# Performance work log

Hardware: AMD Instinct MI355X
Metric: run time of the kernel (lower is better)

Reference implementation:

```python
import jax, jax.numpy as jnp
import numpy as np

N, D, E = 100000, 128, 800000

def setup_inputs() -> dict:
    key = jax.random.key(0)
    k1, k2, k3, k4 = jax.random.split(key, 4)
    z = jax.random.normal(k1, (N, D), dtype=jnp.float32)
    edge_index = jax.random.randint(k2, (2, E), 0, N, dtype=jnp.int64)
    # PyTorch-style init scale for Linear layers (kaiming-uniform-ish via normal is fine for a numeric reference)
    W1 = jax.random.normal(k3, (2 * D, D), dtype=jnp.float32) * (1.0 / np.sqrt(2 * D))
    b1 = jnp.zeros((D,), dtype=jnp.float32)
    W2 = jax.random.normal(k4, (D, 1), dtype=jnp.float32) * (1.0 / np.sqrt(D))
    b2 = jnp.zeros((1,), dtype=jnp.float32)
    return {"z": z, "edge_index": edge_index, "W1": W1, "b1": b1, "W2": W2, "b2": b2}

def reference(z, edge_index, W1, b1, W2, b2):
    # row/col gather of node embeddings
    row, col = edge_index[0], edge_index[1]
    # cat([z[row], z[col]]) @ W1 == z[row] @ W1[:D] + z[col] @ W1[D:]
    # -> avoids materializing the [E, 2D] concatenated tensor
    d = z.shape[1]
    h = z[row] @ W1[:d] + z[col] @ W1[d:] + b1          # [E, D]
    h = jax.nn.relu(h)                                   # Dropout(0.1) is identity in eval mode
    out = h @ W2 + b2                                    # [E, 1]
    return out.squeeze(-1)                               # [E]
```

## Files before the change

### kernel.cpp

```cpp
#include <hip/hip_runtime.h>

#define DDIM 128

typedef __bf16 bf16x8 __attribute__((ext_vector_type(8)));
typedef float  floatx4 __attribute__((ext_vector_type(4)));

__device__ inline unsigned short f2bf(float f) {
    unsigned u = __builtin_bit_cast(unsigned, f);
    u += 0x7fffu + ((u >> 16) & 1u);
    return (unsigned short)(u >> 16);
}

__global__ __launch_bounds__(256) void swizzle_w(
    const float* __restrict__ W1, unsigned short* __restrict__ Wf)
{
    const int id   = blockIdx.x * 256 + threadIdx.x;
    const int f    = id >> 6;
    const int lane = id & 63;
    const int nt = f >> 2, ks = f & 3;
    const int n  = nt * 16 + (lane & 15);
    const int kb = ks * 32 + (lane >> 4) * 8;
    const float* __restrict__ wsrc = (n < DDIM)
        ? (W1 + (size_t)kb * DDIM + n)
        : (W1 + (size_t)(DDIM + kb) * DDIM + (n - DDIM));
    unsigned short frag[8];
    #pragma unroll
    for (int j = 0; j < 8; ++j)
        frag[j] = f2bf(wsrc[(size_t)j * DDIM]);
    *(uint4*)&Wf[(size_t)id * 8] = *(const uint4*)frag;
}

__global__ __launch_bounds__(256, 3) void precompute_uv_mfma_q8(
    const float* __restrict__ z, const unsigned short* __restrict__ Wf,
    const float* __restrict__ b1,
    signed char* __restrict__ U8, signed char* __restrict__ V8,
    float* __restrict__ u_scale, float* __restrict__ v_scale,
    int N)
{
    const int lane = threadIdx.x & 63;
    const int w    = threadIdx.x >> 6;
    const int mrow = lane & 15;
    const int quad = lane >> 4;
    const int m0   = blockIdx.x * 64 + w * 16;

    bf16x8 afrag[4];
    {
        int grow = m0 + mrow; if (grow > N - 1) grow = N - 1;
        const float* zrow = z + (size_t)grow * DDIM;
        #pragma unroll
        for (int ks = 0; ks < 4; ++ks) {
            const int k0 = ks * 32 + quad * 8;
            const float4 x0 = *(const float4*)(zrow + k0);
            const float4 x1 = *(const float4*)(zrow + k0 + 4);
            unsigned short a[8];
            a[0] = f2bf(x0.x); a[1] = f2bf(x0.y); a[2] = f2bf(x0.z); a[3] = f2bf(x0.w);
            a[4] = f2bf(x1.x); a[5] = f2bf(x1.y); a[6] = f2bf(x1.z); a[7] = f2bf(x1.w);
            afrag[ks] = __builtin_bit_cast(bf16x8, *(const uint4*)a);
        }
    }

    #pragma unroll
    for (int half = 0; half < 2; ++half) {
        signed char* __restrict__ dst8 = half ? V8 : U8;
        float*       __restrict__ dscl = half ? v_scale : u_scale;

        float bval[8];
        #pragma unroll
        for (int nt = 0; nt < 8; ++nt)
            bval[nt] = half ? 0.f : b1[nt * 16 + mrow];

        floatx4 acc[8];
        #pragma unroll
        for (int nt = 0; nt < 8; ++nt) acc[nt] = (floatx4){0.f, 0.f, 0.f, 0.f};

        const unsigned short* __restrict__ wbase =
            Wf + ((size_t)half * 32 * 64) * 8 + (size_t)lane * 8;

        #pragma unroll
        for (int ks = 0; ks < 4; ++ks) {
            #pragma unroll
            for (int nt = 0; nt < 8; ++nt) {
                const bf16x8 b = __builtin_bit_cast(bf16x8,
                    *(const uint4*)(wbase + (size_t)((nt * 4 + ks) * 64) * 8));
                acc[nt] = __builtin_amdgcn_mfma_f32_16x16x32_bf16(afrag[ks], b, acc[nt], 0, 0, 0);
            }
        }

        #pragma unroll
        for (int r = 0; r < 4; ++r) {
            float mx = 0.f;
            #pragma unroll
            for (int nt = 0; nt < 8; ++nt)
                mx = fmaxf(mx, fabsf(acc[nt][r] + bval[nt]));
            #pragma unroll
            for (int m = 1; m < 16; m <<= 1)
                mx = fmaxf(mx, __shfl_xor(mx, m, 16));
            mx = fmaxf(mx, 1e-20f);
            const float inv = 127.f / mx;

            unsigned char bytes[8];
            #pragma unroll
            for (int nt = 0; nt < 8; ++nt) {
                const int q = (int)rintf((acc[nt][r] + bval[nt]) * inv);
                bytes[nt] = (unsigned char)(q & 0xff);
            }
            const int grow = m0 + quad * 4 + r;
            if (grow < N) {
                *(unsigned long long*)&dst8[(size_t)grow * DDIM + mrow * 8] =
                    *(const unsigned long long*)bytes;
                if (mrow == 0) dscl[grow] = mx * (1.f / 127.f);
            }
        }
    }
}

__global__ __launch_bounds__(256) void edge_kernel_i8(
    const int* __restrict__ ei,
    const signed char* __restrict__ U8, const signed char* __restrict__ V8,
    const float* __restrict__ u_scale, const float* __restrict__ v_scale,
    const float* __restrict__ W2, const float* __restrict__ b2,
    float* __restrict__ out, int E)
{
    const int t  = threadIdx.x;
    const int p  = t & 15;
    const int g0 = (blockIdx.x * 16 + (t >> 4)) * 4;

    float ww[8];
    #pragma unroll
    for (int j = 0; j < 8; ++j) ww[j] = W2[j * 16 + p];

    if (g0 >= E) return;

    int rows[4], cols[4];
    if (g0 + 3 < E) {
        const int4 r4 = *(const int4*)(ei + g0);
        const int4 c4 = *(const int4*)(ei + (size_t)E + g0);
        rows[0]=r4.x; rows[1]=r4.y; rows[2]=r4.z; rows[3]=r4.w;
        cols[0]=c4.x; cols[1]=c4.y; cols[2]=c4.z; cols[3]=c4.w;
    } else {
        #pragma unroll
        for (int i = 0; i < 4; ++i) {
            const int gi = (g0 + i < E) ? (g0 + i) : (E - 1);
            rows[i] = ei[gi];
            cols[i] = ei[(size_t)E + gi];
        }
    }

    uint2 uu[4], vv[4];
    #pragma unroll
    for (int i = 0; i < 4; ++i)
        uu[i] = *(const uint2*)(U8 + (size_t)rows[i] * DDIM + p * 8);
    #pragma unroll
    for (int i = 0; i < 4; ++i)
        vv[i] = *(const uint2*)(V8 + (size_t)cols[i] * DDIM + p * 8);

    float su[4], sv[4];
    #pragma unroll
    for (int i = 0; i < 4; ++i) { su[i] = u_scale[rows[i]]; sv[i] = v_scale[cols[i]]; }

    const float bias = b2[0];

    #pragma unroll
    for (int i = 0; i < 4; ++i) {
        const signed char* us = (const signed char*)&uu[i];
        const signed char* vs = (const signed char*)&vv[i];
        float s = 0.f;
        #pragma unroll
        for (int j = 0; j < 8; ++j) {
            const float h = fmaf(sv[i], (float)vs[j], su[i] * (float)us[j]);
            s = fmaf(fmaxf(h, 0.f), ww[j], s);
        }
        #pragma unroll
        for (int off = 8; off > 0; off >>= 1)
            s += __shfl_down(s, off, 16);
        if (p == 0 && g0 + i < E) out[g0 + i] = s + bias;
    }
}

__global__ __launch_bounds__(256) void edge_fused_fallback(
    const float* __restrict__ z, const int* __restrict__ ei,
    const float* __restrict__ W1, const float* __restrict__ b1,
    const float* __restrict__ W2, const float* __restrict__ b2,
    float* __restrict__ out, int N, int E)
{
    const int tid  = blockIdx.x * 256 + threadIdx.x;
    const int e    = tid >> 6;
    const int lane = tid & 63;
    if (e >= E) return;

    const int row = ei[e];
    const int col = ei[(size_t)E + e];
    const float* zr = z + (size_t)row * DDIM;
    const float* zc = z + (size_t)col * DDIM;

    float h0 = b1[lane];
    float h1 = b1[lane + 64];
    for (int k = 0; k < DDIM; ++k) {
        const float a = zr[k];
        const float b = zc[k];
        h0 = fmaf(a, W1[k * DDIM + lane],               h0);
        h0 = fmaf(b, W1[(DDIM + k) * DDIM + lane],      h0);
        h1 = fmaf(a, W1[k * DDIM + lane + 64],          h1);
        h1 = fmaf(b, W1[(DDIM + k) * DDIM + lane + 64], h1);
    }
    float s = fmaxf(h0, 0.f) * W2[lane] + fmaxf(h1, 0.f) * W2[lane + 64];
    #pragma unroll
    for (int off = 32; off > 0; off >>= 1)
        s += __shfl_down(s, off, 64);
    if (lane == 0) out[e] = s + b2[0];
}

extern "C" void kernel_launch(void* const* d_in, const int* in_sizes, int n_in,
                              void* d_out, int out_size, void* d_ws, size_t ws_size,
                              hipStream_t stream)
{
    const float* z  = (const float*)d_in[0];
    const int*   ei = (const int*)d_in[1];
    const float* W1 = (const float*)d_in[2];
    const float* b1 = (const float*)d_in[3];
    const float* W2 = (const float*)d_in[4];
    const float* b2 = (const float*)d_in[5];
    float*       out = (float*)d_out;

    const int N = in_sizes[0] / DDIM;
    const int E = in_sizes[1] / 2;

    const size_t n128 = (size_t)N * DDIM;
    const size_t need = 2 * n128 + 2 * (size_t)N * sizeof(float)
                      + 64 * 1024 + 512;
    if (ws_size >= need) {
        signed char* U8 = (signed char*)d_ws;
        signed char* V8 = U8 + n128;
        float* usc = (float*)(((size_t)(V8 + n128) + 255) & ~(size_t)255);
        float* vsc = usc + N;
        unsigned short* Wf = (unsigned short*)(((size_t)(vsc + N) + 255) & ~(size_t)255);

        hipLaunchKernelGGL(swizzle_w, dim3(16), dim3(256), 0, stream, W1, Wf);
        hipLaunchKernelGGL(precompute_uv_mfma_q8, dim3((N + 63) / 64), dim3(256), 0, stream,
                           z, Wf, b1, U8, V8, usc, vsc, N);
        hipLaunchKernelGGL(edge_kernel_i8, dim3((E + 63) / 64), dim3(256), 0, stream,
                           ei, U8, V8, usc, vsc, W2, b2, out, E);
    } else {
        hipLaunchKernelGGL(edge_fused_fallback, dim3((E + 3) / 4), dim3(256), 0, stream,
                           z, ei, W1, b1, W2, b2, out, N, E);
    }
}
```

Before: 146.7 us.

## Switch node precompute to 32x32x16 MFMA tiles with 32 rows per wave

The node-level U/V precompute moves from 16x16x32 bf16 MFMA to 32x32x16 bf16 MFMA. Each wave now handles 32 rows and a block handles 128 nodes. The weight swizzle, the quantized output layout (4 bytes per lane, interleaved columns) and the W2 indexing in the edge kernel are all changed to match. The goal is fewer MFMA issues and weight loads per row, with better reuse of each B fragment. In exchange the grid is halved, accumulators grow to 64 VGPRs, and the per-lane int8 stores become narrower.

```diff
diff --git a/kernel.cpp b/kernel.cpp
--- a/kernel.cpp
+++ b/kernel.cpp
@@ -2,8 +2,8 @@
 
 #define DDIM 128
 
-typedef __bf16 bf16x8 __attribute__((ext_vector_type(8)));
-typedef float  floatx4 __attribute__((ext_vector_type(4)));
+typedef __bf16 bf16x8  __attribute__((ext_vector_type(8)));
+typedef float  floatx16 __attribute__((ext_vector_type(16)));
 
 __device__ inline unsigned short f2bf(float f) {
     unsigned u = __builtin_bit_cast(unsigned, f);
@@ -17,9 +17,9 @@
     const int id   = blockIdx.x * 256 + threadIdx.x;
     const int f    = id >> 6;
     const int lane = id & 63;
-    const int nt = f >> 2, ks = f & 3;
-    const int n  = nt * 16 + (lane & 15);
-    const int kb = ks * 32 + (lane >> 4) * 8;
+    const int ct = f >> 3, s = f & 7;
+    const int n  = ct * 32 + (lane & 31);
+    const int kb = s * 16 + (lane >> 5) * 8;
     const float* __restrict__ wsrc = (n < DDIM)
         ? (W1 + (size_t)kb * DDIM + n)
         : (W1 + (size_t)(DDIM + kb) * DDIM + (n - DDIM));
@@ -39,23 +39,23 @@
 {
     const int lane = threadIdx.x & 63;
     const int w    = threadIdx.x >> 6;
-    const int mrow = lane & 15;
-    const int quad = lane >> 4;
-    const int m0   = blockIdx.x * 64 + w * 16;
-
-    bf16x8 afrag[4];
+    const int c    = lane & 31;
+    const int h    = lane >> 5;
+    const int m0   = blockIdx.x * 128 + w * 32;
+
+    bf16x8 afrag[8];
     {
-        int grow = m0 + mrow; if (grow > N - 1) grow = N - 1;
+        int grow = m0 + c; if (grow > N - 1) grow = N - 1;
         const float* zrow = z + (size_t)grow * DDIM;
         #pragma unroll
-        for (int ks = 0; ks < 4; ++ks) {
-            const int k0 = ks * 32 + quad * 8;
+        for (int s = 0; s < 8; ++s) {
+            const int k0 = s * 16 + h * 8;
             const float4 x0 = *(const float4*)(zrow + k0);
             const float4 x1 = *(const float4*)(zrow + k0 + 4);
             unsigned short a[8];
             a[0] = f2bf(x0.x); a[1] = f2bf(x0.y); a[2] = f2bf(x0.z); a[3] = f2bf(x0.w);
             a[4] = f2bf(x1.x); a[5] = f2bf(x1.y); a[6] = f2bf(x1.z); a[7] = f2bf(x1.w);
-            afrag[ks] = __builtin_bit_cast(bf16x8, *(const uint4*)a);
+            afrag[s] = __builtin_bit_cast(bf16x8, *(const uint4*)a);
         }
     }
 
@@ -64,51 +64,53 @@
         signed char* __restrict__ dst8 = half ? V8 : U8;
         float*       __restrict__ dscl = half ? v_scale : u_scale;
 
-        float bval[8];
-        #pragma unroll
-        for (int nt = 0; nt < 8; ++nt)
-            bval[nt] = half ? 0.f : b1[nt * 16 + mrow];
-
-        floatx4 acc[8];
-        #pragma unroll
-        for (int nt = 0; nt < 8; ++nt) acc[nt] = (floatx4){0.f, 0.f, 0.f, 0.f};
-
-        const unsigned short* __restrict__ wbase =
-            Wf + ((size_t)half * 32 * 64) * 8 + (size_t)lane * 8;
-
-        #pragma unroll
-        for (int ks = 0; ks < 4; ++ks) {
-            #pragma unroll
-            for (int nt = 0; nt < 8; ++nt) {
+        float bval[4];
+        #pragma unroll
+        for (int ct = 0; ct < 4; ++ct)
+            bval[ct] = half ? 0.f : b1[ct * 32 + c];
+
+        floatx16 acc[4];
+        #pragma unroll
+        for (int ct = 0; ct < 4; ++ct)
+            #pragma unroll
+            for (int q = 0; q < 16; ++q) acc[ct][q] = 0.f;
+
+        #pragma unroll
+        for (int s = 0; s < 8; ++s) {
+            #pragma unroll
+            for (int ct = 0; ct < 4; ++ct) {
+                const int f = (half * 4 + ct) * 8 + s;
                 const bf16x8 b = __builtin_bit_cast(bf16x8,
-                    *(const uint4*)(wbase + (size_t)((nt * 4 + ks) * 64) * 8));
-                acc[nt] = __builtin_amdgcn_mfma_f32_16x16x32_bf16(afrag[ks], b, acc[nt], 0, 0, 0);
+                    *(const uint4*)&Wf[((size_t)f * 64 + lane) * 8]);
+                acc[ct] = __builtin_amdgcn_mfma_f32_32x32x16_bf16(afrag[s], b, acc[ct], 0, 0, 0);
             }
         }
 
         #pragma unroll
-        for (int r = 0; r < 4; ++r) {
-            float mx = 0.f;
-            #pragma unroll
-            for (int nt = 0; nt < 8; ++nt)
-                mx = fmaxf(mx, fabsf(acc[nt][r] + bval[nt]));
-            #pragma unroll
-            for (int m = 1; m < 16; m <<= 1)
-                mx = fmaxf(mx, __shfl_xor(mx, m, 16));
+        for (int q = 0; q < 16; ++q) {
+            float v[4];
+            #pragma unroll
+            for (int ct = 0; ct < 4; ++ct) v[ct] = acc[ct][q] + bval[ct];
+
+            float mx = fmaxf(fmaxf(fabsf(v[0]), fabsf(v[1])),
+                             fmaxf(fabsf(v[2]), fabsf(v[3])));
+            #pragma unroll
+            for (int m = 1; m < 32; m <<= 1)
+                mx = fmaxf(mx, __shfl_xor(mx, m, 32));
             mx = fmaxf(mx, 1e-20f);
             const float inv = 127.f / mx;
 
-            unsigned char bytes[8];
-            #pragma unroll
-            for (int nt = 0; nt < 8; ++nt) {
-                const int q = (int)rintf((acc[nt][r] + bval[nt]) * inv);
-                bytes[nt] = (unsigned char)(q & 0xff);
-            }
-            const int grow = m0 + quad * 4 + r;
+            unsigned char bytes[4];
+            #pragma unroll
+            for (int ct = 0; ct < 4; ++ct)
+                bytes[ct] = (unsigned char)(((int)rintf(v[ct] * inv)) & 0xff);
+
+            const int lrow = (q & 3) + 8 * (q >> 2) + 4 * h;
+            const int grow = m0 + lrow;
             if (grow < N) {
-                *(unsigned long long*)&dst8[(size_t)grow * DDIM + mrow * 8] =
-                    *(const unsigned long long*)bytes;
-                if (mrow == 0) dscl[grow] = mx * (1.f / 127.f);
+                *(unsigned int*)&dst8[(size_t)grow * DDIM + c * 4] =
+                    *(const unsigned int*)bytes;
+                if (c == 0) dscl[grow] = mx * (1.f / 127.f);
             }
         }
     }
@@ -127,7 +129,7 @@
 
     float ww[8];
     #pragma unroll
-    for (int j = 0; j < 8; ++j) ww[j] = W2[j * 16 + p];
+    for (int j = 0; j < 8; ++j) ww[j] = W2[(j & 3) * 32 + 2 * p + (j >> 2)];
 
     if (g0 >= E) return;
 
@@ -236,7 +238,7 @@
         unsigned short* Wf = (unsigned short*)(((size_t)(vsc + N) + 255) & ~(size_t)255);
 
         hipLaunchKernelGGL(swizzle_w, dim3(16), dim3(256), 0, stream, W1, Wf);
-        hipLaunchKernelGGL(precompute_uv_mfma_q8, dim3((N + 63) / 64), dim3(256), 0, stream,
+        hipLaunchKernelGGL(precompute_uv_mfma_q8, dim3((N + 127) / 128), dim3(256), 0, stream,
                            z, Wf, b1, U8, V8, usc, vsc, N);
         hipLaunchKernelGGL(edge_kernel_i8, dim3((E + 63) / 64), dim3(256), 0, stream,
                            ei, U8, V8, usc, vsc, W2, b2, out, E);
```

Result: slower. 152.6 us (+4.0%).

## Make node precompute kernel persistent with prefetch of next chunk's z rows

Applied to the files above, without the earlier changes.

The per-node U/V precompute kernel becomes a grid-stride persistent kernel with 512 blocks. Each block prefetches the next 64-row chunk of z into registers while it runs the MFMA and quantisation for the current chunk. The half loop is no longer unrolled and the bias loads are hoisted out of the loop. The aim is to hide global load latency for z behind compute, at the cost of more register pressure from the prefetch buffers, which may lower occupancy.

```diff
diff --git a/kernel.cpp b/kernel.cpp
--- a/kernel.cpp
+++ b/kernel.cpp
@@ -19,7 +19,7 @@
     const int lane = id & 63;
     const int nt = f >> 2, ks = f & 3;
     const int n  = nt * 16 + (lane & 15);
-    const int kb = ks * 32 + (lane >> 4) * 8;
+    const int kb = ks * 32 + ((lane >> 4) & 3) * 8;
     const float* __restrict__ wsrc = (n < DDIM)
         ? (W1 + (size_t)kb * DDIM + n)
         : (W1 + (size_t)(DDIM + kb) * DDIM + (n - DDIM));
@@ -35,82 +35,116 @@
     const float* __restrict__ b1,
     signed char* __restrict__ U8, signed char* __restrict__ V8,
     float* __restrict__ u_scale, float* __restrict__ v_scale,
-    int N)
+    int N, int nchunks)
 {
     const int lane = threadIdx.x & 63;
     const int w    = threadIdx.x >> 6;
     const int mrow = lane & 15;
     const int quad = lane >> 4;
-    const int m0   = blockIdx.x * 64 + w * 16;
-
-    bf16x8 afrag[4];
+
+    float bu[8];
+    #pragma unroll
+    for (int nt = 0; nt < 8; ++nt) bu[nt] = b1[nt * 16 + mrow];
+
+    int chunk = blockIdx.x;
+    if (chunk >= nchunks) return;
+
+    const int koff = quad * 8;
+
+    float4 raw[8];
     {
-        int grow = m0 + mrow; if (grow > N - 1) grow = N - 1;
+        int grow = chunk * 64 + w * 16 + mrow; if (grow > N - 1) grow = N - 1;
         const float* zrow = z + (size_t)grow * DDIM;
         #pragma unroll
         for (int ks = 0; ks < 4; ++ks) {
-            const int k0 = ks * 32 + quad * 8;
-            const float4 x0 = *(const float4*)(zrow + k0);
-            const float4 x1 = *(const float4*)(zrow + k0 + 4);
+            raw[ks * 2]     = *(const float4*)(zrow + ks * 32 + koff);
+            raw[ks * 2 + 1] = *(const float4*)(zrow + ks * 32 + koff + 4);
+        }
+    }
+
+    while (true) {
+        const int next = chunk + gridDim.x;
+        const bool have_next = next < nchunks;
+
+        bf16x8 afrag[4];
+        #pragma unroll
+        for (int ks = 0; ks < 4; ++ks) {
+            const float4 x0 = raw[ks * 2], x1 = raw[ks * 2 + 1];
             unsigned short a[8];
             a[0] = f2bf(x0.x); a[1] = f2bf(x0.y); a[2] = f2bf(x0.z); a[3] = f2bf(x0.w);
             a[4] = f2bf(x1.x); a[5] = f2bf(x1.y); a[6] = f2bf(x1.z); a[7] = f2bf(x1.w);
             afrag[ks] = __builtin_bit_cast(bf16x8, *(const uint4*)a);
         }
-    }
-
-    #pragma unroll
-    for (int half = 0; half < 2; ++half) {
-        signed char* __restrict__ dst8 = half ? V8 : U8;
-        float*       __restrict__ dscl = half ? v_scale : u_scale;
-
-        float bval[8];
-        #pragma unroll
-        for (int nt = 0; nt < 8; ++nt)
-            bval[nt] = half ? 0.f : b1[nt * 16 + mrow];
-
-        floatx4 acc[8];
-        #pragma unroll
-        for (int nt = 0; nt < 8; ++nt) acc[nt] = (floatx4){0.f, 0.f, 0.f, 0.f};
-
-        const unsigned short* __restrict__ wbase =
-            Wf + ((size_t)half * 32 * 64) * 8 + (size_t)lane * 8;
-
-        #pragma unroll
-        for (int ks = 0; ks < 4; ++ks) {
-            #pragma unroll
-            for (int nt = 0; nt < 8; ++nt) {
-                const bf16x8 b = __builtin_bit_cast(bf16x8,
-                    *(const uint4*)(wbase + (size_t)((nt * 4 + ks) * 64) * 8));
-                acc[nt] = __builtin_amdgcn_mfma_f32_16x16x32_bf16(afrag[ks], b, acc[nt], 0, 0, 0);
+
+        float4 raw2[8];
+        if (have_next) {
+            int grow = next * 64 + w * 16 + mrow; if (grow > N - 1) grow = N - 1;
+            const float* zrow = z + (size_t)grow * DDIM;
+            #pragma unroll
+            for (int ks = 0; ks < 4; ++ks) {
+                raw2[ks * 2]     = *(const float4*)(zrow + ks * 32 + koff);
+                raw2[ks * 2 + 1] = *(const float4*)(zrow + ks * 32 + koff + 4);
             }
         }
 
-        #pragma unroll
-        for (int r = 0; r < 4; ++r) {
-            float mx = 0.f;
-            #pragma unroll
-            for (int nt = 0; nt < 8; ++nt)
-                mx = fmaxf(mx, fabsf(acc[nt][r] + bval[nt]));
-            #pragma unroll
-            for (int m = 1; m < 16; m <<= 1)
-                mx = fmaxf(mx, __shfl_xor(mx, m, 16));
-            mx = fmaxf(mx, 1e-20f);
-            const float inv = 127.f / mx;
-
-            unsigned char bytes[8];
-            #pragma unroll
-            for (int nt = 0; nt < 8; ++nt) {
-                const int q = (int)rintf((acc[nt][r] + bval[nt]) * inv);
-                bytes[nt] = (unsigned char)(q & 0xff);
+        const int m0 = chunk * 64 + w * 16;
+
+        #pragma unroll 1
+        for (int half = 0; half < 2; ++half) {
+            signed char* __restrict__ dst8 = half ? V8 : U8;
+            float*       __restrict__ dscl = half ? v_scale : u_scale;
+
+            floatx4 acc[8];
+            #pragma unroll
+            for (int nt = 0; nt < 8; ++nt) acc[nt] = (floatx4){0.f, 0.f, 0.f, 0.f};
+
+            const unsigned short* __restrict__ wbase =
+                Wf + ((size_t)half * 32 * 64) * 8 + (size_t)lane * 8;
+
+            #pragma unroll
+            for (int ks = 0; ks < 4; ++ks) {
+                #pragma unroll
+                for (int nt = 0; nt < 8; ++nt) {
+                    const bf16x8 b = __builtin_bit_cast(bf16x8,
+                        *(const uint4*)(wbase + (size_t)((nt * 4 + ks) * 64) * 8));
+                    acc[nt] = __builtin_amdgcn_mfma_f32_16x16x32_bf16(afrag[ks], b, acc[nt], 0, 0, 0);
+                }
             }
-            const int grow = m0 + quad * 4 + r;
-            if (grow < N) {
-                *(unsigned long long*)&dst8[(size_t)grow * DDIM + mrow * 8] =
-                    *(const unsigned long long*)bytes;
-                if (mrow == 0) dscl[grow] = mx * (1.f / 127.f);
+
+            #pragma unroll
+            for (int r = 0; r < 4; ++r) {
+                float v[8];
+                #pragma unroll
+                for (int nt = 0; nt < 8; ++nt)
+                    v[nt] = half ? acc[nt][r] : (acc[nt][r] + bu[nt]);
+
+                float mx = 0.f;
+                #pragma unroll
+                for (int nt = 0; nt < 8; ++nt) mx = fmaxf(mx, fabsf(v[nt]));
+                #pragma unroll
+                for (int m = 1; m < 16; m <<= 1)
+                    mx = fmaxf(mx, __shfl_xor(mx, m, 16));
+                mx = fmaxf(mx, 1e-20f);
+                const float inv = 127.f / mx;
+
+                unsigned char bytes[8];
+                #pragma unroll
+                for (int nt = 0; nt < 8; ++nt)
+                    bytes[nt] = (unsigned char)(((int)rintf(v[nt] * inv)) & 0xff);
+
+                const int grow = m0 + quad * 4 + r;
+                if (grow < N) {
+                    *(unsigned long long*)&dst8[(size_t)grow * DDIM + mrow * 8] =
+                        *(const unsigned long long*)bytes;
+                    if (mrow == 0) dscl[grow] = mx * (1.f / 127.f);
+                }
             }
         }
+
+        if (!have_next) break;
+        #pragma unroll
+        for (int i = 0; i < 8; ++i) raw[i] = raw2[i];
+        chunk = next;
     }
 }
 
@@ -235,9 +269,10 @@
         float* vsc = usc + N;
         unsigned short* Wf = (unsigned short*)(((size_t)(vsc + N) + 255) & ~(size_t)255);
 
+        const int nchunks = (N + 63) / 64;
         hipLaunchKernelGGL(swizzle_w, dim3(16), dim3(256), 0, stream, W1, Wf);
-        hipLaunchKernelGGL(precompute_uv_mfma_q8, dim3((N + 63) / 64), dim3(256), 0, stream,
-                           z, Wf, b1, U8, V8, usc, vsc, N);
+        hipLaunchKernelGGL(precompute_uv_mfma_q8, dim3(512), dim3(256), 0, stream,
+                           z, Wf, b1, U8, V8, usc, vsc, N, nchunks);
         hipLaunchKernelGGL(edge_kernel_i8, dim3((E + 63) / 64), dim3(256), 0, stream,
                            ei, U8, V8, usc, vsc, W2, b2, out, E);
     } else {
```

Measured after the change: 148.5 us. Within noise of the previous version (+1.2%).
